# Optimization experiments

Measured on AMD Instinct MI355X. Metric: run time of the kernel, lower is better.

## Reference

```python
import jax, jax.numpy as jnp
import numpy as np

N = 100000
E = 1600000
D_IN = 128
D_HID = 128
D_OUT = 128


def setup_inputs() -> dict:
    key = jax.random.key(0)
    ks = jax.random.split(key, 12)
    x = jax.random.normal(ks[0], (N, D_IN), dtype=jnp.float32)
    edge_index = jax.random.randint(ks[1], (2, E), 0, N, dtype=jnp.int32)
    def lin(k, fan_in, fan_out):
        s = 1.0 / np.sqrt(fan_in)
        return jax.random.uniform(k, (fan_in, fan_out), jnp.float32, -s, s)
    dims = [(D_IN, D_HID), (D_HID, D_HID), (D_HID, D_OUT)]
    inp = {"x": x, "edge_index": edge_index}
    for i, (fi, fo) in enumerate(dims):
        inp[f"Wl{i}"] = lin(ks[2 + 3 * i], fi, fo)
        inp[f"Wr{i}"] = lin(ks[3 + 3 * i], fi, fo)
        inp[f"b{i}"] = jnp.zeros((fo,), jnp.float32)
    return inp


def _sage_conv(h, row, col, Wl, Wr, b):
    # mean aggregation over incoming neighbors: out[i] = mean_{j->i} h[j]
    n = h.shape[0]
    agg = jax.ops.segment_sum(h[col], row, num_segments=n)  # [N, d]
    deg = jax.ops.segment_sum(jnp.ones_like(row, dtype=h.dtype), row, num_segments=n)
    agg = agg / jnp.maximum(deg, 1.0)[:, None]
    return agg @ Wl + b + h @ Wr


def reference(x, edge_index, Wl0, Wr0, b0, Wl1, Wr1, b1, Wl2, Wr2, b2):
    row, col = edge_index[0], edge_index[1]  # dst, src
    h1 = jax.nn.relu(_sage_conv(x, row, col, Wl0, Wr0, b0))   # dropout is no-op in eval
    h2 = jax.nn.relu(_sage_conv(h1, row, col, Wl1, Wr1, b1))
    h3 = jax.nn.relu(_sage_conv(h2, row, col, Wl2, Wr2, b2))
    return (h1, h2, h3)
```

## Files before the change

kernel.cpp:

```cpp
#include <hip/hip_runtime.h>

#define NN 100000
#define NE 1600000
#define DD 128
#define BM 64
#define NPB 256
#define NBUCK 391
#define ECHUNK 8192
#define NBLK_PART 196
#define CAP 8192
#define CVX_BLK 800
#define CVW_BLK 384

typedef __attribute__((ext_vector_type(2))) float f32x2;
typedef __attribute__((ext_vector_type(4))) float f32x4;
typedef __attribute__((ext_vector_type(8))) short bf16x8;

__device__ inline unsigned short f2bf(float f) {
    unsigned int x = __builtin_bit_cast(unsigned int, f);
    unsigned int r = x + 0x7fffu + ((x >> 16) & 1u);
    return (unsigned short)(r >> 16);
}
__device__ inline unsigned int packbf(float a, float b) {
    return (unsigned int)f2bf(a) | ((unsigned int)f2bf(b) << 16);
}
__device__ inline unsigned int pk_fp8x4(float a, float b, float c, float d) {
    int v = 0;
    v = __builtin_amdgcn_cvt_pk_fp8_f32(a, b, v, false);
    v = __builtin_amdgcn_cvt_pk_fp8_f32(c, d, v, true);
    return (unsigned int)v;
}
__device__ inline f32x2 upk_fp8_lo(unsigned int v) {
    return __builtin_amdgcn_cvt_pk_f32_fp8((int)v, false);
}
__device__ inline f32x2 upk_fp8_hi(unsigned int v) {
    return __builtin_amdgcn_cvt_pk_f32_fp8((int)v, true);
}

__device__ inline void load_g2l_16(const void* gsrc, void* ldst) {
    __builtin_amdgcn_global_load_lds(
        (const __attribute__((address_space(1))) void*)(uintptr_t)gsrc,
        (__attribute__((address_space(3))) void*)(uintptr_t)ldst,
        16, 0, 0);
}


__global__ __launch_bounds__(256) void prep_kernel(
    const float* __restrict__ x, unsigned short* __restrict__ xb,
    unsigned int* __restrict__ xf8,
    const float* __restrict__ w0, const float* __restrict__ w1,
    const float* __restrict__ w2, const float* __restrict__ w3,
    const float* __restrict__ w4, const float* __restrict__ w5,
    unsigned short* __restrict__ wtall,
    const int* __restrict__ row, int* __restrict__ gcnt) {
    __shared__ int cnt[NBUCK];
    const int b = blockIdx.x;
    if (b < CVX_BLK) {
        int i = b * 256 + threadIdx.x;
        const int n4 = NN * DD / 4;
        for (; i < n4; i += CVX_BLK * 256) {
            float4 v = reinterpret_cast<const float4*>(x)[i];
            ushort4 o;
            o.x = f2bf(v.x); o.y = f2bf(v.y); o.z = f2bf(v.z); o.w = f2bf(v.w);
            reinterpret_cast<ushort4*>(xb)[i] = o;
            xf8[i] = pk_fp8x4(v.x, v.y, v.z, v.w);
        }
    } else if (b < CVX_BLK + CVW_BLK) {
        int t = (b - CVX_BLK) * 256 + threadIdx.x;
        int i = t >> 14;
        int r = t & 16383;
        const float* W = (i == 0) ? w0 : (i == 1) ? w1 : (i == 2) ? w2
                        : (i == 3) ? w3 : (i == 4) ? w4 : w5;
        int c = r >> 7, k = r & 127;
        wtall[t] = f2bf(W[k * DD + c]);
    } else {
        for (int i = threadIdx.x; i < NBUCK; i += 256) cnt[i] = 0;
        __syncthreads();
        int base = (b - CVX_BLK - CVW_BLK) * ECHUNK;
        int end = base + ECHUNK; if (end > NE) end = NE;
        for (int i = base + threadIdx.x; i < end; i += 256)
            atomicAdd(&cnt[row[i] >> 8], 1);
        __syncthreads();
        for (int i = threadIdx.x; i < NBUCK; i += 256) {
            int c = cnt[i];
            if (c) atomicAdd(&gcnt[i], c);
        }
    }
}


__global__ __launch_bounds__(512) void bucket_scan(const int* __restrict__ gcnt,
                                                   int* __restrict__ gbase) {
    __shared__ int sm[512];
    int t = threadIdx.x;
    sm[t] = (t < NBUCK) ? gcnt[t] : 0;
    __syncthreads();
    for (int off = 1; off < 512; off <<= 1) {
        int add = (t >= off) ? sm[t - off] : 0;
        __syncthreads();
        sm[t] += add;
        __syncthreads();
    }
    if (t < NBUCK) gbase[t + 1] = sm[t];
    if (t == 0) gbase[0] = 0;
}

__global__ __launch_bounds__(256) void bucket_scatter(const int* __restrict__ row,
                                                      const int* __restrict__ col,
                                                      const int* __restrict__ gbase,
                                                      int* __restrict__ gcursor,
                                                      uint2* __restrict__ ebuf) {
    __shared__ int cnt[NBUCK];
    __shared__ int base[NBUCK];
    for (int i = threadIdx.x; i < NBUCK; i += 256) cnt[i] = 0;
    __syncthreads();
    int cbase = blockIdx.x * ECHUNK;
    int cend = cbase + ECHUNK; if (cend > NE) cend = NE;
    for (int i = cbase + threadIdx.x; i < cend; i += 256)
        atomicAdd(&cnt[row[i] >> 8], 1);
    __syncthreads();
    for (int i = threadIdx.x; i < NBUCK; i += 256) {
        int c = cnt[i];
        cnt[i] = 0;
        base[i] = c ? (gbase[i] + atomicAdd(&gcursor[i], c)) : 0;
    }
    __syncthreads();
    for (int i = cbase + threadIdx.x; i < cend; i += 256) {
        int r = row[i], c = col[i];
        int b = r >> 8;
        int k = atomicAdd(&cnt[b], 1);
        ebuf[base[b] + k] = uint2{(unsigned)r, (unsigned)c};
    }
}

__global__ __launch_bounds__(256) void csr_build(const uint2* __restrict__ ebuf,
                                                 const int* __restrict__ gbase,
                                                 int* __restrict__ offs,
                                                 int* __restrict__ csr_col) {
    __shared__ int dcnt[NPB];
    __shared__ int doff[NPB];
    __shared__ int sm[NPB];
    __shared__ int stage[CAP];
    const int b = blockIdx.x;
    const int es = gbase[b], ee = gbase[b + 1];
    const int m = ee - es;
    const int t = threadIdx.x;
    const int nbase = b * NPB;

    dcnt[t] = 0;
    __syncthreads();
    for (int i = es + t; i < ee; i += 256) {
        int ln = (int)ebuf[i].x - nbase;
        atomicAdd(&dcnt[ln], 1);
    }
    __syncthreads();
    sm[t] = dcnt[t];
    __syncthreads();
    for (int off = 1; off < 256; off <<= 1) {
        int add = (t >= off) ? sm[t - off] : 0;
        __syncthreads();
        sm[t] += add;
        __syncthreads();
    }
    doff[t] = sm[t] - dcnt[t];
    int node = nbase + t;
    if (node < NN) offs[node + 1] = es + sm[t];
    if (b == 0 && t == 0) offs[0] = 0;
    dcnt[t] = 0;
    __syncthreads();

    if (m <= CAP) {
        for (int i = es + t; i < ee; i += 256) {
            uint2 e = ebuf[i];
            int ln = (int)e.x - nbase;
            int k = atomicAdd(&dcnt[ln], 1);
            stage[doff[ln] + k] = (int)e.y;
        }
        __syncthreads();
        for (int i = t; i < m; i += 256) csr_col[es + i] = stage[i];
    } else {
        for (int i = es + t; i < ee; i += 256) {
            uint2 e = ebuf[i];
            int ln = (int)e.x - nbase;
            int k = atomicAdd(&dcnt[ln], 1);
            csr_col[es + doff[ln] + k] = (int)e.y;
        }
    }
}


__global__ __launch_bounds__(256) void fused_layer(
    const unsigned short* __restrict__ hb,
    const unsigned int* __restrict__ f8,
    const int* __restrict__ offs, const int* __restrict__ csr_col,
    const unsigned short* __restrict__ WlT, const unsigned short* __restrict__ WrT,
    const float* __restrict__ bias, float* __restrict__ out,
    unsigned short* __restrict__ hbn, unsigned int* __restrict__ f8n) {
    __shared__ uint4 smem4[2048];
    char* AldsB = (char*)smem4;
    char* HldsB = AldsB + 16384;
    const int row0 = blockIdx.x * BM;
    const int tid = threadIdx.x;
    const int w = tid >> 6, l = tid & 63;

    const char* Hsrc = (const char*)(hb + (size_t)row0 * DD);
#pragma unroll
    for (int j = 0; j < 4; ++j) {
        int base = w * 4096 + j * 1024;
        int doff = base + l * 16;
        int soff = doff ^ (((doff >> 8) & 7) << 4);
        if (row0 + (doff >> 8) < NN) load_g2l_16(Hsrc + soff, HldsB + base);
    }

    const int g16 = tid >> 4, lane = tid & 15;
    for (int i = 0; i < 4; ++i) {
        const int rloc = g16 * 4 + i;
        const int node = row0 + rloc;
        f32x2 a0 = {0.f, 0.f}, a1 = {0.f, 0.f}, a2 = {0.f, 0.f}, a3 = {0.f, 0.f};
        float inv = 0.0f;
        if (node < NN) {
            int s = offs[node], e = offs[node + 1];
            int p = s;
            for (; p + 8 <= e; p += 8) {
                uint2 v[8];
#pragma unroll
                for (int q = 0; q < 8; ++q) {
                    int c = csr_col[p + q];
                    v[q] = *reinterpret_cast<const uint2*>(f8 + (size_t)c * 32 + lane * 2);
                }
#pragma unroll
                for (int q = 0; q < 8; ++q) {
                    a0 += upk_fp8_lo(v[q].x);
                    a1 += upk_fp8_hi(v[q].x);
                    a2 += upk_fp8_lo(v[q].y);
                    a3 += upk_fp8_hi(v[q].y);
                }
            }
            for (; p < e; ++p) {
                int c = csr_col[p];
                uint2 v = *reinterpret_cast<const uint2*>(f8 + (size_t)c * 32 + lane * 2);
                a0 += upk_fp8_lo(v.x);
                a1 += upk_fp8_hi(v.x);
                a2 += upk_fp8_lo(v.y);
                a3 += upk_fp8_hi(v.y);
            }
            inv = (e > s) ? (1.0f / (float)(e - s)) : 0.0f;
        }
        uint4 o;
        o.x = packbf(a0[0] * inv, a0[1] * inv);
        o.y = packbf(a1[0] * inv, a1[1] * inv);
        o.z = packbf(a2[0] * inv, a2[1] * inv);
        o.w = packbf(a3[0] * inv, a3[1] * inv);
        int off = (rloc << 8) + ((lane * 16) ^ ((rloc & 7) << 4));
        *reinterpret_cast<uint4*>(AldsB + off) = o;
    }
    __syncthreads();

    const int wr = w & 1, wc = w >> 1;
    const int lrow = l & 15, lg = l >> 4;

    f32x4 acc[2][4];
#pragma unroll
    for (int m = 0; m < 2; ++m)
#pragma unroll
        for (int n = 0; n < 4; ++n) acc[m][n] = (f32x4){0.f, 0.f, 0.f, 0.f};

    float bv[4];
#pragma unroll
    for (int n = 0; n < 4; ++n) bv[n] = bias[wc * 64 + n * 16 + lrow];

#pragma unroll
    for (int kb = 0; kb < 4; ++kb) {
        const int kbyte = kb * 64 + lg * 16;
        bf16x8 aA[2], aH[2];
#pragma unroll
        for (int m = 0; m < 2; ++m) {
            int rloc = wr * 32 + m * 16 + lrow;
            int off = (rloc << 8) + kbyte;
            off ^= (rloc & 7) << 4;
            aA[m] = *reinterpret_cast<const bf16x8*>(AldsB + off);
            aH[m] = *reinterpret_cast<const bf16x8*>(HldsB + off);
        }
        bf16x8 bL[4], bR[4];
#pragma unroll
        for (int n = 0; n < 4; ++n) {
            size_t woff = ((size_t)(wc * 64 + n * 16 + lrow) << 7) + kb * 32 + lg * 8;
            bL[n] = *reinterpret_cast<const bf16x8*>(WlT + woff);
            bR[n] = *reinterpret_cast<const bf16x8*>(WrT + woff);
        }
#pragma unroll
        for (int m = 0; m < 2; ++m)
#pragma unroll
            for (int n = 0; n < 4; ++n) {
                acc[m][n] = __builtin_amdgcn_mfma_f32_16x16x32_bf16(aA[m], bL[n], acc[m][n], 0, 0, 0);
                acc[m][n] = __builtin_amdgcn_mfma_f32_16x16x32_bf16(aH[m], bR[n], acc[m][n], 0, 0, 0);
            }
    }

    __syncthreads();
    float* otile = (float*)smem4;
#pragma unroll
    for (int m = 0; m < 2; ++m) {
        int rb = wr * 32 + m * 16 + lg * 4;
#pragma unroll
        for (int n = 0; n < 4; ++n) {
            int c = wc * 64 + n * 16 + lrow;
#pragma unroll
            for (int j = 0; j < 4; ++j)
                otile[(rb + j) * DD + c] = fmaxf(acc[m][n][j] + bv[n], 0.0f);
        }
    }
    __syncthreads();
    const f32x4* t4 = (const f32x4*)smem4;
#pragma unroll
    for (int it = 0; it < 8; ++it) {
        int idx = it * 256 + tid;
        int r = idx >> 5;
        int gr = row0 + r;
        if (gr < NN) {
            f32x4 v = t4[idx];
            __builtin_nontemporal_store(v, (f32x4*)out + (size_t)gr * 32 + (idx & 31));
            if (hbn) {
                uint2 pk;
                pk.x = packbf(v[0], v[1]);
                pk.y = packbf(v[2], v[3]);
                *((uint2*)hbn + (size_t)gr * 32 + (idx & 31)) = pk;
                f8n[(size_t)gr * 32 + (idx & 31)] = pk_fp8x4(v[0], v[1], v[2], v[3]);
            }
        }
    }
}

extern "C" void kernel_launch(void* const* d_in, const int* in_sizes, int n_in,
                              void* d_out, int out_size, void* d_ws, size_t ws_size,
                              hipStream_t stream) {
    const float* x = (const float*)d_in[0];
    const int* ei = (const int*)d_in[1];
    const int* row = ei;
    const int* col = ei + NE;
    const float* Wl[3] = {(const float*)d_in[2], (const float*)d_in[5], (const float*)d_in[8]};
    const float* Wr[3] = {(const float*)d_in[3], (const float*)d_in[6], (const float*)d_in[9]};
    const float* bb[3] = {(const float*)d_in[4], (const float*)d_in[7], (const float*)d_in[10]};
    float* out = (float*)d_out;

    char* ws = (char*)d_ws;
    auto carve = [&](size_t bytes) {
        char* p = ws;
        ws += (bytes + 255) & ~(size_t)255;
        return p;
    };
    unsigned short* buf0 = (unsigned short*)carve((size_t)NN * DD * 2);
    unsigned short* buf1 = (unsigned short*)carve((size_t)NN * DD * 2);
    unsigned int* f8a = (unsigned int*)carve((size_t)NN * DD);
    unsigned int* f8b = (unsigned int*)carve((size_t)NN * DD);
    unsigned short* wtall = (unsigned short*)carve((size_t)6 * DD * DD * 2);
    int* gcnt    = (int*)carve((size_t)2 * NBUCK * sizeof(int));
    int* gcursor = gcnt + NBUCK;
    int* gbase   = (int*)carve((size_t)(NBUCK + 1) * sizeof(int));
    int* offs    = (int*)carve((size_t)(NN + 1) * sizeof(int));
    uint2* ebuf  = (uint2*)carve((size_t)NE * sizeof(uint2));
    int* csr_col = (int*)carve((size_t)NE * sizeof(int));

    hipMemsetAsync(gcnt, 0, (size_t)2 * NBUCK * sizeof(int), stream);

    prep_kernel<<<CVX_BLK + CVW_BLK + NBLK_PART, 256, 0, stream>>>(
        x, buf0, f8a, Wl[0], Wr[0], Wl[1], Wr[1], Wl[2], Wr[2], wtall, row, gcnt);
    bucket_scan<<<1, 512, 0, stream>>>(gcnt, gbase);
    bucket_scatter<<<NBLK_PART, 256, 0, stream>>>(row, col, gbase, gcursor, ebuf);
    csr_build<<<NBUCK, 256, 0, stream>>>(ebuf, gbase, offs, csr_col);

    const int ngrid = (NN + BM - 1) / BM;

    unsigned short* hin = buf0;
    unsigned short* hout = buf1;
    unsigned int* f8in = f8a;
    unsigned int* f8out = f8b;
    for (int lyr = 0; lyr < 3; ++lyr) {
        float* o = out + (size_t)lyr * NN * DD;
        fused_layer<<<ngrid, 256, 0, stream>>>(
            hin, f8in, offs, csr_col,
            wtall + (size_t)2 * lyr * DD * DD, wtall + (size_t)(2 * lyr + 1) * DD * DD,
            bb[lyr], o,
            (lyr < 2) ? hout : (unsigned short*)nullptr,
            (lyr < 2) ? f8out : (unsigned int*)nullptr);
        unsigned short* t = hin; hin = hout; hout = t;
        unsigned int* t8 = f8in; f8in = f8out; f8out = t8;
    }
}
```

Before: 318.9 us.

## Halve fused layer LDS, load self features to registers, pack edge buffer

The self-feature tile is no longer staged in LDS through async global-to-LDS loads. Each wave now loads its MFMA A-operand fragments for H directly into registers. The neighbor gather uses 8-lane groups with 16-byte fp8 loads over two rows per group instead of 16-lane groups with 8-byte loads. The output epilogue is split into two 32-row halves so LDS drops from 32KB to 16KB, which is meant to allow more resident blocks. The edge bucket buffer is packed into one 32-bit word per edge (col<<8 | local row), halving its traffic, at the cost of more registers in the fused kernel and an extra barrier round in the epilogue.

Measured after the change: 314.2 us. No clear change (-1.5%).

```diff
diff --git a/kernel.cpp b/kernel.cpp
--- a/kernel.cpp
+++ b/kernel.cpp
@@ -35,13 +35,6 @@
 }
 __device__ inline f32x2 upk_fp8_hi(unsigned int v) {
     return __builtin_amdgcn_cvt_pk_f32_fp8((int)v, true);
-}
-
-__device__ inline void load_g2l_16(const void* gsrc, void* ldst) {
-    __builtin_amdgcn_global_load_lds(
-        (const __attribute__((address_space(1))) void*)(uintptr_t)gsrc,
-        (__attribute__((address_space(3))) void*)(uintptr_t)ldst,
-        16, 0, 0);
 }
 
 
@@ -109,7 +102,7 @@
                                                       const int* __restrict__ col,
                                                       const int* __restrict__ gbase,
                                                       int* __restrict__ gcursor,
-                                                      uint2* __restrict__ ebuf) {
+                                                      unsigned int* __restrict__ ebuf) {
     __shared__ int cnt[NBUCK];
     __shared__ int base[NBUCK];
     for (int i = threadIdx.x; i < NBUCK; i += 256) cnt[i] = 0;
@@ -129,11 +122,11 @@
         int r = row[i], c = col[i];
         int b = r >> 8;
         int k = atomicAdd(&cnt[b], 1);
-        ebuf[base[b] + k] = uint2{(unsigned)r, (unsigned)c};
-    }
-}
-
-__global__ __launch_bounds__(256) void csr_build(const uint2* __restrict__ ebuf,
+        ebuf[base[b] + k] = ((unsigned)c << 8) | ((unsigned)r & 255u);
+    }
+}
+
+__global__ __launch_bounds__(256) void csr_build(const unsigned int* __restrict__ ebuf,
                                                  const int* __restrict__ gbase,
                                                  int* __restrict__ offs,
                                                  int* __restrict__ csr_col) {
@@ -150,7 +143,7 @@
     dcnt[t] = 0;
     __syncthreads();
     for (int i = es + t; i < ee; i += 256) {
-        int ln = (int)ebuf[i].x - nbase;
+        int ln = (int)(ebuf[i] & 255u);
         atomicAdd(&dcnt[ln], 1);
     }
     __syncthreads();
@@ -171,19 +164,19 @@
 
     if (m <= CAP) {
         for (int i = es + t; i < ee; i += 256) {
-            uint2 e = ebuf[i];
-            int ln = (int)e.x - nbase;
+            unsigned e = ebuf[i];
+            int ln = (int)(e & 255u);
             int k = atomicAdd(&dcnt[ln], 1);
-            stage[doff[ln] + k] = (int)e.y;
+            stage[doff[ln] + k] = (int)(e >> 8);
         }
         __syncthreads();
         for (int i = t; i < m; i += 256) csr_col[es + i] = stage[i];
     } else {
         for (int i = es + t; i < ee; i += 256) {
-            uint2 e = ebuf[i];
-            int ln = (int)e.x - nbase;
+            unsigned e = ebuf[i];
+            int ln = (int)(e & 255u);
             int k = atomicAdd(&dcnt[ln], 1);
-            csr_col[es + doff[ln] + k] = (int)e.y;
+            csr_col[es + doff[ln] + k] = (int)(e >> 8);
         }
     }
 }
@@ -196,68 +189,75 @@
     const unsigned short* __restrict__ WlT, const unsigned short* __restrict__ WrT,
     const float* __restrict__ bias, float* __restrict__ out,
     unsigned short* __restrict__ hbn, unsigned int* __restrict__ f8n) {
-    __shared__ uint4 smem4[2048];
+    __shared__ uint4 smem4[1024];
     char* AldsB = (char*)smem4;
-    char* HldsB = AldsB + 16384;
     const int row0 = blockIdx.x * BM;
     const int tid = threadIdx.x;
     const int w = tid >> 6, l = tid & 63;
-
-    const char* Hsrc = (const char*)(hb + (size_t)row0 * DD);
-#pragma unroll
-    for (int j = 0; j < 4; ++j) {
-        int base = w * 4096 + j * 1024;
-        int doff = base + l * 16;
-        int soff = doff ^ (((doff >> 8) & 7) << 4);
-        if (row0 + (doff >> 8) < NN) load_g2l_16(Hsrc + soff, HldsB + base);
-    }
-
-    const int g16 = tid >> 4, lane = tid & 15;
-    for (int i = 0; i < 4; ++i) {
-        const int rloc = g16 * 4 + i;
+    const int wr = w & 1, wc = w >> 1;
+    const int lrow = l & 15, lg = l >> 4;
+
+    bf16x8 aH[2][4];
+#pragma unroll
+    for (int m = 0; m < 2; ++m) {
+        int gr = row0 + wr * 32 + m * 16 + lrow;
+        if (gr >= NN) gr = NN - 1;
+        const unsigned short* hrow = hb + (size_t)gr * DD;
+#pragma unroll
+        for (int kb = 0; kb < 4; ++kb)
+            aH[m][kb] = *reinterpret_cast<const bf16x8*>(hrow + kb * 32 + lg * 8);
+    }
+
+    const int grp = tid >> 3, lane = tid & 7;
+    const uint4* f84 = reinterpret_cast<const uint4*>(f8);
+#pragma unroll
+    for (int i = 0; i < 2; ++i) {
+        const int rloc = grp * 2 + i;
         const int node = row0 + rloc;
-        f32x2 a0 = {0.f, 0.f}, a1 = {0.f, 0.f}, a2 = {0.f, 0.f}, a3 = {0.f, 0.f};
+        f32x2 a[8];
+#pragma unroll
+        for (int k = 0; k < 8; ++k) a[k] = (f32x2){0.f, 0.f};
         float inv = 0.0f;
         if (node < NN) {
             int s = offs[node], e = offs[node + 1];
             int p = s;
             for (; p + 8 <= e; p += 8) {
-                uint2 v[8];
+                uint4 v[8];
+#pragma unroll
+                for (int q = 0; q < 8; ++q)
+                    v[q] = f84[(size_t)csr_col[p + q] * 8 + lane];
 #pragma unroll
                 for (int q = 0; q < 8; ++q) {
-                    int c = csr_col[p + q];
-                    v[q] = *reinterpret_cast<const uint2*>(f8 + (size_t)c * 32 + lane * 2);
+                    a[0] += upk_fp8_lo(v[q].x); a[1] += upk_fp8_hi(v[q].x);
+                    a[2] += upk_fp8_lo(v[q].y); a[3] += upk_fp8_hi(v[q].y);
+                    a[4] += upk_fp8_lo(v[q].z); a[5] += upk_fp8_hi(v[q].z);
+                    a[6] += upk_fp8_lo(v[q].w); a[7] += upk_fp8_hi(v[q].w);
                 }
-#pragma unroll
-                for (int q = 0; q < 8; ++q) {
-                    a0 += upk_fp8_lo(v[q].x);
-                    a1 += upk_fp8_hi(v[q].x);
-                    a2 += upk_fp8_lo(v[q].y);
-                    a3 += upk_fp8_hi(v[q].y);
-                }
             }
             for (; p < e; ++p) {
-                int c = csr_col[p];
-                uint2 v = *reinterpret_cast<const uint2*>(f8 + (size_t)c * 32 + lane * 2);
-                a0 += upk_fp8_lo(v.x);
-                a1 += upk_fp8_hi(v.x);
-                a2 += upk_fp8_lo(v.y);
-                a3 += upk_fp8_hi(v.y);
+                uint4 v = f84[(size_t)csr_col[p] * 8 + lane];
+                a[0] += upk_fp8_lo(v.x); a[1] += upk_fp8_hi(v.x);
+                a[2] += upk_fp8_lo(v.y); a[3] += upk_fp8_hi(v.y);
+                a[4] += upk_fp8_lo(v.z); a[5] += upk_fp8_hi(v.z);
+                a[6] += upk_fp8_lo(v.w); a[7] += upk_fp8_hi(v.w);
             }
             inv = (e > s) ? (1.0f / (float)(e - s)) : 0.0f;
         }
-        uint4 o;
-        o.x = packbf(a0[0] * inv, a0[1] * inv);
-        o.y = packbf(a1[0] * inv, a1[1] * inv);
-        o.z = packbf(a2[0] * inv, a2[1] * inv);
-        o.w = packbf(a3[0] * inv, a3[1] * inv);
-        int off = (rloc << 8) + ((lane * 16) ^ ((rloc & 7) << 4));
-        *reinterpret_cast<uint4*>(AldsB + off) = o;
-    }
-    __syncthreads();
-
-    const int wr = w & 1, wc = w >> 1;
-    const int lrow = l & 15, lg = l >> 4;
+        uint4 o0, o1;
+        o0.x = packbf(a[0][0] * inv, a[0][1] * inv);
+        o0.y = packbf(a[1][0] * inv, a[1][1] * inv);
+        o0.z = packbf(a[2][0] * inv, a[2][1] * inv);
+        o0.w = packbf(a[3][0] * inv, a[3][1] * inv);
+        o1.x = packbf(a[4][0] * inv, a[4][1] * inv);
+        o1.y = packbf(a[5][0] * inv, a[5][1] * inv);
+        o1.z = packbf(a[6][0] * inv, a[6][1] * inv);
+        o1.w = packbf(a[7][0] * inv, a[7][1] * inv);
+        const int sw = (rloc & 7) << 4;
+        const int rbase = rloc << 8;
+        *reinterpret_cast<uint4*>(AldsB + rbase + ((lane * 32) ^ sw)) = o0;
+        *reinterpret_cast<uint4*>(AldsB + rbase + ((lane * 32 + 16) ^ sw)) = o1;
+    }
+    __syncthreads();
 
     f32x4 acc[2][4];
 #pragma unroll
@@ -272,14 +272,13 @@
 #pragma unroll
     for (int kb = 0; kb < 4; ++kb) {
         const int kbyte = kb * 64 + lg * 16;
-        bf16x8 aA[2], aH[2];
+        bf16x8 aA[2];
 #pragma unroll
         for (int m = 0; m < 2; ++m) {
             int rloc = wr * 32 + m * 16 + lrow;
             int off = (rloc << 8) + kbyte;
             off ^= (rloc & 7) << 4;
             aA[m] = *reinterpret_cast<const bf16x8*>(AldsB + off);
-            aH[m] = *reinterpret_cast<const bf16x8*>(HldsB + off);
         }
         bf16x8 bL[4], bR[4];
 #pragma unroll
@@ -293,41 +292,47 @@
 #pragma unroll
             for (int n = 0; n < 4; ++n) {
                 acc[m][n] = __builtin_amdgcn_mfma_f32_16x16x32_bf16(aA[m], bL[n], acc[m][n], 0, 0, 0);
-                acc[m][n] = __builtin_amdgcn_mfma_f32_16x16x32_bf16(aH[m], bR[n], acc[m][n], 0, 0, 0);
+                acc[m][n] = __builtin_amdgcn_mfma_f32_16x16x32_bf16(aH[m][kb], bR[n], acc[m][n], 0, 0, 0);
             }
     }
 
     __syncthreads();
     float* otile = (float*)smem4;
 #pragma unroll
-    for (int m = 0; m < 2; ++m) {
-        int rb = wr * 32 + m * 16 + lg * 4;
-#pragma unroll
-        for (int n = 0; n < 4; ++n) {
-            int c = wc * 64 + n * 16 + lrow;
-#pragma unroll
-            for (int j = 0; j < 4; ++j)
-                otile[(rb + j) * DD + c] = fmaxf(acc[m][n][j] + bv[n], 0.0f);
-        }
-    }
-    __syncthreads();
-    const f32x4* t4 = (const f32x4*)smem4;
-#pragma unroll
-    for (int it = 0; it < 8; ++it) {
-        int idx = it * 256 + tid;
-        int r = idx >> 5;
-        int gr = row0 + r;
-        if (gr < NN) {
-            f32x4 v = t4[idx];
-            __builtin_nontemporal_store(v, (f32x4*)out + (size_t)gr * 32 + (idx & 31));
-            if (hbn) {
-                uint2 pk;
-                pk.x = packbf(v[0], v[1]);
-                pk.y = packbf(v[2], v[3]);
-                *((uint2*)hbn + (size_t)gr * 32 + (idx & 31)) = pk;
-                f8n[(size_t)gr * 32 + (idx & 31)] = pk_fp8x4(v[0], v[1], v[2], v[3]);
-            }
-        }
+    for (int half = 0; half < 2; ++half) {
+        if (wr == half) {
+#pragma unroll
+            for (int m = 0; m < 2; ++m) {
+                int rb = m * 16 + lg * 4;
+#pragma unroll
+                for (int n = 0; n < 4; ++n) {
+                    int c = wc * 64 + n * 16 + lrow;
+#pragma unroll
+                    for (int j = 0; j < 4; ++j)
+                        otile[(rb + j) * DD + c] = fmaxf(acc[m][n][j] + bv[n], 0.0f);
+                }
+            }
+        }
+        __syncthreads();
+        const f32x4* t4 = (const f32x4*)smem4;
+#pragma unroll
+        for (int it = 0; it < 4; ++it) {
+            int idx = it * 256 + tid;
+            int r = idx >> 5;
+            int gr = row0 + half * 32 + r;
+            if (gr < NN) {
+                f32x4 v = t4[idx];
+                __builtin_nontemporal_store(v, (f32x4*)out + (size_t)gr * 32 + (idx & 31));
+                if (hbn) {
+                    uint2 pk;
+                    pk.x = packbf(v[0], v[1]);
+                    pk.y = packbf(v[2], v[3]);
+                    *((uint2*)hbn + (size_t)gr * 32 + (idx & 31)) = pk;
+                    f8n[(size_t)gr * 32 + (idx & 31)] = pk_fp8x4(v[0], v[1], v[2], v[3]);
+                }
+            }
+        }
+        __syncthreads();
     }
 }
 
@@ -358,7 +363,7 @@
     int* gcursor = gcnt + NBUCK;
     int* gbase   = (int*)carve((size_t)(NBUCK + 1) * sizeof(int));
     int* offs    = (int*)carve((size_t)(NN + 1) * sizeof(int));
-    uint2* ebuf  = (uint2*)carve((size_t)NE * sizeof(uint2));
+    unsigned int* ebuf = (unsigned int*)carve((size_t)NE * sizeof(unsigned int));
     int* csr_col = (int*)carve((size_t)NE * sizeof(int));
 
     hipMemsetAsync(gcnt, 0, (size_t)2 * NBUCK * sizeof(int), stream);
```
